# Kernel tuning notes

Measured on AMD Instinct MI355X. Metric: run time of the kernel, lower is better.

The kernel has to match this reference:

```python
import jax, jax.numpy as jnp
import numpy as np
from jax import lax

FX, FY = 518.857, 519.469   # NYU-v2 depth intrinsics (cx/cy unused by forward)
B, H, W = 8, 479, 639       # TRAIN_CROP_SIZE = [W, H]; H+1, W+1 divisible by 4
P = 8                       # even PATCH_SIZE -> box-filter output is [H+1, W+1]
EPS = 1e-6


def _coords():
    # u_u0 = x - W/2, v_v0 = y - H/2, broadcast over [B,1,H,W]
    u = jnp.arange(W, dtype=jnp.float32)[None, None, None, :] - W / 2.0
    v = jnp.arange(H, dtype=jnp.float32)[None, None, :, None] - H / 2.0
    return u, v


def _surface_normal(xyz):
    # xyz: [H, W, 3] -> normals [H, W, 3]
    x, y, z = xyz[..., 0], xyz[..., 1], xyz[..., 2]
    # 9 box-filtered moments in a single depthwise conv (the original does 9 conv2d calls)
    mom = jnp.stack([x * x, x * y, x * z, y * y, y * z, z * z, x, y, z], 0)[None]  # [1,9,H,W]
    kern = jnp.ones((9, 1, P, P), xyz.dtype)
    s = lax.conv_general_dilated(mom, kern, (1, 1), [(P // 2, P // 2)] * 2,
                                 feature_group_count=9)[0]  # [9, H+1, W+1]
    xx, xy, xz, yy, yz, zz, xs, ys, zs = s
    ATA = jnp.stack([xx, xy, xz, xy, yy, yz, xz, yz, zz], -1)  # [H+1, W+1, 9]
    Hp, Wp = ATA.shape[0], ATA.shape[1]
    ATA = ATA.reshape(Hp, Wp, 3, 3) + EPS * jnp.eye(3, dtype=xyz.dtype)
    AT1 = jnp.stack([xs, ys, zs], -1)[..., None]  # [H+1, W+1, 3, 1]
    # original loops over 4x4 sub-patches with overlap=0 -> equivalent full-grid solve
    n = jnp.linalg.solve(ATA, AT1)                # [H+1, W+1, 3, 1]
    n = n / jnp.sqrt(jnp.sum(n * n, axis=2, keepdims=True))
    n = n[:-1, :-1, :, 0]                         # [H, W, 3]
    # orient toward camera: flip where dot(n, xyz) > 0
    flip = jnp.sum(n * xyz, axis=2, keepdims=True) > 0
    return jnp.where(flip, -n, n)


def _fit_normals(depth):
    # depth: [B,1,H,W] -> surface normals [B,3,H,W], zeroed where depth <= 0
    u, v = _coords()
    x = u * depth / FX
    y = v * depth / FY
    xyz = jnp.concatenate([x, y, depth], 1).transpose(0, 2, 3, 1)  # [B,H,W,3]
    sn = jax.vmap(_surface_normal)(xyz).transpose(0, 3, 1, 2)      # [B,3,H,W]
    return jnp.where(depth > 0, sn, 0.0)


def setup_inputs() -> dict:
    key = jax.random.key(0)
    k1, k2 = jax.random.split(key)
    prediction = jax.random.uniform(k1, (B, 1, H, W), jnp.float32)
    gt = jax.random.uniform(k2, (B, 1, H, W), jnp.float32)
    return {"prediction": prediction, "gt": gt}


def reference(prediction, gt):
    return jnp.mean(jnp.abs(_fit_normals(prediction) - _fit_normals(gt)))
```

## Files before the change

### kernel.cpp

```cpp
#include <hip/hip_runtime.h>

#define HH 479
#define WW 639
#define BATCH 8
#define NACC 64


__device__ __forceinline__ void solve_normal(
    float xx, float xy, float xz, float yy, float yz, float zz,
    float xs, float ys, float zs,
    float a_c, float b_c, float d0,
    float* nx, float* ny, float* nz)
{
    const float EPSV = 1e-6f;
    const float inv64 = 1.0f / 64.0f;
    float hx = xs * inv64, hy = ys * inv64, hz = zs * inv64;
    float cxx = fmaf(-hx, xs, xx) + EPSV;
    float cxy = fmaf(-hx, ys, xy);
    float cxz = fmaf(-hx, zs, xz);
    float cyy = fmaf(-hy, ys, yy) + EPSV;
    float cyz = fmaf(-hy, zs, yz);
    float czz = fmaf(-hz, zs, zz) + EPSV;
    float c00 = fmaf(cyy, czz, -cyz * cyz);
    float c01 = fmaf(cxz, cyz, -cxy * czz);
    float c02 = fmaf(cxy, cyz, -cxz * cyy);
    float c11 = fmaf(cxx, czz, -cxz * cxz);
    float c12 = fmaf(cxy, cxz, -cxx * cyz);
    float c22 = fmaf(cxx, cyy, -cxy * cxy);
    float m0 = fmaf(c00, xs, fmaf(c01, ys, c02 * zs));
    float m1 = fmaf(c01, xs, fmaf(c11, ys, c12 * zs));
    float m2 = fmaf(c02, xs, fmaf(c12, ys, c22 * zs));
    float g  = fmaf(m0, a_c, fmaf(m1, b_c, m2));
    float inv = rsqrtf(fmaf(m0, m0, fmaf(m1, m1, m2 * m2)));
    if (g > 0.0f) inv = -inv;
    if (!(d0 > 0.0f)) inv = 0.0f;
    *nx = m0 * inv; *ny = m1 * inv; *nz = m2 * inv;
}

__global__ __launch_bounds__(256, 4)
void ppal_main(const float* __restrict__ pred, const float* __restrict__ gt,
               double* __restrict__ acc)
{
    const int tx = threadIdx.x;
    const int ty = threadIdx.y;
    const int tid = ty * 16 + tx;
    const int j0 = blockIdx.x * 16;
    const int i0 = blockIdx.y * 16;
    const int b  = blockIdx.z;

    const float invFX = 1.0f / 518.857f;
    const float invFY = 1.0f / 519.469f;

    __shared__ float sd[2][23 * 24];
    __shared__ float cs[2][384][6];

    const float* src0 = pred + (size_t)b * (HH * WW);
    const float* src1 = gt   + (size_t)b * (HH * WW);
    for (int idx = tid; idx < 23 * 24; idx += 256) {
        int lr = idx / 24, lc = idx - lr * 24;
        int r = i0 - 4 + lr, c = j0 - 4 + lc;
        bool ok = (lc < 23) && (r >= 0) && (r < HH) && (c >= 0) && (c < WW);
        int off = r * WW + c;
        sd[0][idx] = ok ? src0[off] : 0.0f;
        sd[1][idx] = ok ? src1[off] : 0.0f;
    }
    __syncthreads();

    for (int t = tid; t < 384; t += 256) {
        int i = t / 24;
        int c = t - i * 24;
        float S1[2] = {0.f, 0.f}, Sb[2] = {0.f, 0.f}, Sbb[2] = {0.f, 0.f};
        float T1[2] = {0.f, 0.f}, Tb[2] = {0.f, 0.f};
#pragma unroll
        for (int dr = 0; dr < 8; ++dr) {
            float bv = ((float)(i0 + i - 4 + dr) - 239.5f) * invFY;
#pragma unroll
            for (int k = 0; k < 2; ++k) {
                float d  = sd[k][(i + dr) * 24 + c];
                float bd = bv * d;
                T1[k] += d;
                Tb[k] += bd;
                S1[k]  = fmaf(d,  d,  S1[k]);
                Sb[k]  = fmaf(bd, d,  Sb[k]);
                Sbb[k] = fmaf(bd, bd, Sbb[k]);
            }
        }
#pragma unroll
        for (int k = 0; k < 2; ++k) {
            float* e = cs[k][t];
            *(float2*)(e)     = make_float2(S1[k], Sb[k]);
            *(float2*)(e + 2) = make_float2(Sbb[k], T1[k]);
            e[4] = Tb[k];
        }
    }
    __syncthreads();

    const int i = i0 + ty, j = j0 + tx;
    const bool valid = (i < HH) && (j < WW);

    float contrib = 0.0f;
    if (valid) {
        float aa[8], a2[8];
#pragma unroll
        for (int dc = 0; dc < 8; ++dc) {
            float a = ((float)(j - 4 + dc) - 319.5f) * invFX;
            aa[dc] = a;
            a2[dc] = a * a;
        }
        float bc = ((float)i - 239.5f) * invFY;
        const int ebase = ty * 24 + tx;

        float n2[2][3];
#pragma unroll
        for (int k = 0; k < 2; ++k) {
            float xx = 0.f, xy = 0.f, xz = 0.f, yy = 0.f, yz = 0.f, zz = 0.f;
            float xs = 0.f, ys = 0.f, zs = 0.f;
#pragma unroll
            for (int dc = 0; dc < 8; ++dc) {
                const float* e = cs[k][ebase + dc];
                float2 p01 = *(const float2*)(e);
                float2 p23 = *(const float2*)(e + 2);
                float  tb  = e[4];
                zz += p01.x;  yz += p01.y;  yy += p23.x;
                zs += p23.y;  ys += tb;
                xz = fmaf(aa[dc], p01.x, xz);
                xy = fmaf(aa[dc], p01.y, xy);
                xs = fmaf(aa[dc], p23.y, xs);
                xx = fmaf(a2[dc], p01.x, xx);
            }
            float d0 = sd[k][(ty + 4) * 24 + (tx + 4)];
            solve_normal(xx, xy, xz, yy, yz, zz, xs, ys, zs,
                         aa[4], bc, d0, &n2[k][0], &n2[k][1], &n2[k][2]);
        }
        contrib = fabsf(n2[0][0] - n2[1][0])
                + fabsf(n2[0][1] - n2[1][1])
                + fabsf(n2[0][2] - n2[1][2]);
    }

    float v = contrib;
#pragma unroll
    for (int off = 32; off > 0; off >>= 1) v += __shfl_down(v, off, 64);
    __shared__ float wsum[4];
    int wid = tid >> 6, lane = tid & 63;
    if (lane == 0) wsum[wid] = v;
    __syncthreads();
    if (tid == 0) {
        double bs = (double)wsum[0] + (double)wsum[1] + (double)wsum[2] + (double)wsum[3];
        int slot = (blockIdx.x + 40 * blockIdx.y + 1200 * blockIdx.z) & (NACC - 1);
        atomicAdd(&acc[slot], bs);
    }
}

__global__ void ppal_finalize(const double* __restrict__ acc, float* __restrict__ out)
{
    int lane = threadIdx.x;
    double v = acc[lane];
#pragma unroll
    for (int off = 32; off > 0; off >>= 1) v += __shfl_down(v, off, 64);
    if (lane == 0)
        out[0] = (float)(v * (1.0 / 7345944.0));
}

extern "C" void kernel_launch(void* const* d_in, const int* in_sizes, int n_in,
                              void* d_out, int out_size, void* d_ws, size_t ws_size,
                              hipStream_t stream)
{
    const float* pred = (const float*)d_in[0];
    const float* gt   = (const float*)d_in[1];
    float* out  = (float*)d_out;
    double* acc = (double*)d_ws;

    hipMemsetAsync(acc, 0, NACC * sizeof(double), stream);

    dim3 grid((WW + 15) / 16, (HH + 15) / 16, BATCH);
    dim3 block(16, 16);
    ppal_main<<<grid, block, 0, stream>>>(pred, gt, acc);
    ppal_finalize<<<1, 64, 0, stream>>>(acc, out);
}
```

Baseline: 112.6 us.

## Compute two adjacent output columns per thread sharing the horizontal box sum

Each block now covers a 16x32 tile, so every thread produces two horizontally adjacent normals. The 7 shared column-sum entries are accumulated once and each output adds its own edge column. This halves the block count and the redundant per-pixel horizontal accumulation and shared-memory reads, and lowers the halo overhead per output. The cost is more registers per thread and fewer total threads.

```diff
diff --git a/kernel.cpp b/kernel.cpp
--- a/kernel.cpp
+++ b/kernel.cpp
@@ -44,31 +44,31 @@
     const int tx = threadIdx.x;
     const int ty = threadIdx.y;
     const int tid = ty * 16 + tx;
-    const int j0 = blockIdx.x * 16;
+    const int j0 = blockIdx.x * 32;
     const int i0 = blockIdx.y * 16;
     const int b  = blockIdx.z;
 
     const float invFX = 1.0f / 518.857f;
     const float invFY = 1.0f / 519.469f;
 
-    __shared__ float sd[2][23 * 24];
-    __shared__ float cs[2][384][6];
+    __shared__ float sd[2][23 * 40];
+    __shared__ float cs[2][624 * 6];
 
     const float* src0 = pred + (size_t)b * (HH * WW);
     const float* src1 = gt   + (size_t)b * (HH * WW);
-    for (int idx = tid; idx < 23 * 24; idx += 256) {
-        int lr = idx / 24, lc = idx - lr * 24;
+    for (int idx = tid; idx < 23 * 40; idx += 256) {
+        int lr = idx / 40, lc = idx - lr * 40;
         int r = i0 - 4 + lr, c = j0 - 4 + lc;
-        bool ok = (lc < 23) && (r >= 0) && (r < HH) && (c >= 0) && (c < WW);
+        bool ok = (lc < 39) && (r >= 0) && (r < HH) && (c >= 0) && (c < WW);
         int off = r * WW + c;
         sd[0][idx] = ok ? src0[off] : 0.0f;
         sd[1][idx] = ok ? src1[off] : 0.0f;
     }
     __syncthreads();
 
-    for (int t = tid; t < 384; t += 256) {
-        int i = t / 24;
-        int c = t - i * 24;
+    for (int t = tid; t < 624; t += 256) {
+        int i = t / 39;
+        int c = t - i * 39;
         float S1[2] = {0.f, 0.f}, Sb[2] = {0.f, 0.f}, Sbb[2] = {0.f, 0.f};
         float T1[2] = {0.f, 0.f}, Tb[2] = {0.f, 0.f};
 #pragma unroll
@@ -76,7 +76,7 @@
             float bv = ((float)(i0 + i - 4 + dr) - 239.5f) * invFY;
 #pragma unroll
             for (int k = 0; k < 2; ++k) {
-                float d  = sd[k][(i + dr) * 24 + c];
+                float d  = sd[k][(i + dr) * 40 + c];
                 float bd = bv * d;
                 T1[k] += d;
                 Tb[k] += bd;
@@ -87,7 +87,7 @@
         }
 #pragma unroll
         for (int k = 0; k < 2; ++k) {
-            float* e = cs[k][t];
+            float* e = &cs[k][6 * t];
             *(float2*)(e)     = make_float2(S1[k], Sb[k]);
             *(float2*)(e + 2) = make_float2(Sbb[k], T1[k]);
             e[4] = Tb[k];
@@ -95,46 +95,72 @@
     }
     __syncthreads();
 
-    const int i = i0 + ty, j = j0 + tx;
-    const bool valid = (i < HH) && (j < WW);
-
+    const int i  = i0 + ty;
+    const int jl = j0 + 2 * tx;
+    const bool valid0 = (i < HH);
+    const bool valid1 = (i < HH) && (jl + 1 < WW);
+
+    float aw[9], aw2[9];
+#pragma unroll
+    for (int m = 0; m < 9; ++m) {
+        float a = ((float)(jl + m - 4) - 319.5f) * invFX;
+        aw[m] = a;
+        aw2[m] = a * a;
+    }
+    float bc = ((float)i - 239.5f) * invFY;
+    const int ebase = ty * 39 + 2 * tx;
+
+    float n0A[3], n1A[3];
     float contrib = 0.0f;
-    if (valid) {
-        float aa[8], a2[8];
-#pragma unroll
-        for (int dc = 0; dc < 8; ++dc) {
-            float a = ((float)(j - 4 + dc) - 319.5f) * invFX;
-            aa[dc] = a;
-            a2[dc] = a * a;
-        }
-        float bc = ((float)i - 239.5f) * invFY;
-        const int ebase = ty * 24 + tx;
-
-        float n2[2][3];
-#pragma unroll
-        for (int k = 0; k < 2; ++k) {
-            float xx = 0.f, xy = 0.f, xz = 0.f, yy = 0.f, yz = 0.f, zz = 0.f;
-            float xs = 0.f, ys = 0.f, zs = 0.f;
-#pragma unroll
-            for (int dc = 0; dc < 8; ++dc) {
-                const float* e = cs[k][ebase + dc];
-                float2 p01 = *(const float2*)(e);
-                float2 p23 = *(const float2*)(e + 2);
-                float  tb  = e[4];
-                zz += p01.x;  yz += p01.y;  yy += p23.x;
-                zs += p23.y;  ys += tb;
-                xz = fmaf(aa[dc], p01.x, xz);
-                xy = fmaf(aa[dc], p01.y, xy);
-                xs = fmaf(aa[dc], p23.y, xs);
-                xx = fmaf(a2[dc], p01.x, xx);
-            }
-            float d0 = sd[k][(ty + 4) * 24 + (tx + 4)];
+#pragma unroll
+    for (int k = 0; k < 2; ++k) {
+        float Sxx = 0.f, Sxy = 0.f, Sxz = 0.f, Syy = 0.f, Syz = 0.f, Szz = 0.f;
+        float Sxs = 0.f, Sys = 0.f, Szs = 0.f;
+#pragma unroll
+        for (int m = 1; m < 8; ++m) {
+            const float* e = &cs[k][6 * (ebase + m)];
+            float2 p01 = *(const float2*)(e);
+            float2 p23 = *(const float2*)(e + 2);
+            float  tb  = e[4];
+            Szz += p01.x;  Syz += p01.y;  Syy += p23.x;
+            Szs += p23.y;  Sys += tb;
+            Sxz = fmaf(aw[m],  p01.x, Sxz);
+            Sxy = fmaf(aw[m],  p01.y, Sxy);
+            Sxs = fmaf(aw[m],  p23.y, Sxs);
+            Sxx = fmaf(aw2[m], p01.x, Sxx);
+        }
+
+        float nn[2][3];
+#pragma unroll
+        for (int p = 0; p < 2; ++p) {
+            int m = (p == 0) ? 0 : 8;
+            const float* e = &cs[k][6 * (ebase + m)];
+            float2 p01 = *(const float2*)(e);
+            float2 p23 = *(const float2*)(e + 2);
+            float  tb  = e[4];
+            float xx = fmaf(aw2[m], p01.x, Sxx);
+            float xy = fmaf(aw[m],  p01.y, Sxy);
+            float xz = fmaf(aw[m],  p01.x, Sxz);
+            float yy = Syy + p23.x;
+            float yz = Syz + p01.y;
+            float zz = Szz + p01.x;
+            float xs = fmaf(aw[m],  p23.y, Sxs);
+            float ys = Sys + tb;
+            float zs = Szs + p23.y;
+            float d0 = sd[k][(ty + 4) * 40 + (2 * tx + p + 4)];
             solve_normal(xx, xy, xz, yy, yz, zz, xs, ys, zs,
-                         aa[4], bc, d0, &n2[k][0], &n2[k][1], &n2[k][2]);
-        }
-        contrib = fabsf(n2[0][0] - n2[1][0])
-                + fabsf(n2[0][1] - n2[1][1])
-                + fabsf(n2[0][2] - n2[1][2]);
+                         aw[4 + p], bc, d0, &nn[p][0], &nn[p][1], &nn[p][2]);
+        }
+        if (k == 0) {
+            n0A[0] = nn[0][0]; n0A[1] = nn[0][1]; n0A[2] = nn[0][2];
+            n1A[0] = nn[1][0]; n1A[1] = nn[1][1]; n1A[2] = nn[1][2];
+        } else {
+            float c0 = fabsf(n0A[0] - nn[0][0]) + fabsf(n0A[1] - nn[0][1])
+                     + fabsf(n0A[2] - nn[0][2]);
+            float c1 = fabsf(n1A[0] - nn[1][0]) + fabsf(n1A[1] - nn[1][1])
+                     + fabsf(n1A[2] - nn[1][2]);
+            contrib = (valid0 ? c0 : 0.0f) + (valid1 ? c1 : 0.0f);
+        }
     }
 
     float v = contrib;
@@ -146,7 +172,7 @@
     __syncthreads();
     if (tid == 0) {
         double bs = (double)wsum[0] + (double)wsum[1] + (double)wsum[2] + (double)wsum[3];
-        int slot = (blockIdx.x + 40 * blockIdx.y + 1200 * blockIdx.z) & (NACC - 1);
+        int slot = (blockIdx.x + 20 * blockIdx.y + 600 * blockIdx.z) & (NACC - 1);
         atomicAdd(&acc[slot], bs);
     }
 }
@@ -172,7 +198,7 @@
 
     hipMemsetAsync(acc, 0, NACC * sizeof(double), stream);
 
-    dim3 grid((WW + 15) / 16, (HH + 15) / 16, BATCH);
+    dim3 grid(20, 30, BATCH);
     dim3 block(16, 16);
     ppal_main<<<grid, block, 0, stream>>>(pred, gt, acc);
     ppal_finalize<<<1, 64, 0, stream>>>(acc, out);
```

Result: faster. 100.7 us (-10.6%).
